# Optimization experiments

Hardware: AMD Instinct MI355X
Metric: run time of the kernel (lower is better)

The kernel has to match this reference:

```python
import jax, jax.numpy as jnp
import numpy as np

VOCAB = 100000
D = 128
B = 256
L = 2048  # leaves per tree (power of two -> complete binary tree)


def setup_inputs() -> dict:
    key = jax.random.key(0)
    k1, k2, k3, k4 = jax.random.split(key, 4)
    word_ids = jax.random.randint(k1, (B, L), 0, VOCAB)
    embedding = jax.random.normal(k2, (VOCAB, D), dtype=jnp.float32) * 0.1
    # torch nn.Linear(2*D, D): weight [D, 2*D], bias [D]
    W = jax.random.normal(k3, (D, 2 * D), dtype=jnp.float32) * (1.0 / np.sqrt(2 * D))
    b = jax.random.normal(k4, (D,), dtype=jnp.float32) * 0.01
    return {"word_ids": word_ids, "embedding": embedding, "W": W, "b": b}


def reference(word_ids, embedding, W, b):
    # Leaves: embedding lookup for every leaf of every tree. [B, L, D]
    x = embedding[word_ids]
    # Internal nodes, batched by depth: each level combines adjacent pairs
    # via linear(concat(left, right)). log2(L) levels (static unroll).
    while x.shape[1] > 1:
        left = x[:, 0::2, :]   # [B, n/2, D]
        right = x[:, 1::2, :]  # [B, n/2, D]
        pair = jnp.concatenate([left, right], axis=-1)  # [B, n/2, 2D]
        x = jnp.einsum('bnd,od->bno', pair, W) + b      # [B, n/2, D]
    return x[:, 0, :]  # root result per tree, [B, D]
```

## Files before the change

kernel.cpp:

```cpp
#include <hip/hip_runtime.h>


typedef __bf16 bf16x8 __attribute__((ext_vector_type(8)));
typedef float f32x4 __attribute__((ext_vector_type(4)));

#define STRIDE 136

__device__ __forceinline__ unsigned short bf16rne(float x) {
    union { float f; unsigned int u; } v; v.f = x;
    unsigned int u = v.u;
    u += 0x7fffu + ((u >> 16) & 1u);
    return (unsigned short)(u >> 16);
}

__global__ void pack_w_kernel(const float* __restrict__ W,
                              unsigned short* __restrict__ wpack) {
    const int f = blockIdx.x;
    const int tid = threadIdx.x;
    const int wv = tid >> 6, l = tid & 63;
    const int nl = f >> 3, kk = f & 7;
    const int o = ((wv << 1) + nl) * 16 + (l & 15);
    const int d = kk * 32 + ((l >> 4) << 3);
    const float* src = W + o * 256 + d;
    unsigned short h[8];
#pragma unroll
    for (int j = 0; j < 8; ++j) h[j] = bf16rne(src[j]);
    uint4* dst = (uint4*)(wpack + (size_t)(f * 256 + tid) * 8);
    *dst = *(const uint4*)h;
}

__global__ __launch_bounds__(256) void tree64_kernel(
    const int* __restrict__ wid, const float* __restrict__ emb,
    const unsigned short* __restrict__ wpack, const float* __restrict__ bias,
    unsigned short* __restrict__ yout)
{
    __shared__ __align__(16) unsigned short buf[2][64 * STRIDE];
    __shared__ int ids[64];
    const int tid = threadIdx.x;
    const int blk = blockIdx.x;
    const int batch = blk >> 5;
    const int sub = blk & 31;
    const int wv = tid >> 6;
    const int ln = tid & 63;
    const int q = ln >> 4;
    const int lm = ln & 15;

    if (tid < 64) ids[tid] = wid[batch * 2048 + sub * 64 + tid];

    bf16x8 wf[16];
    const bf16x8* wp = (const bf16x8*)wpack;
#pragma unroll
    for (int f = 0; f < 16; ++f) wf[f] = wp[f * 256 + tid];

    float bval[2];
    bval[0] = bias[(2 * wv + 0) * 16 + lm];
    bval[1] = bias[(2 * wv + 1) * 16 + lm];

    __syncthreads();

#pragma unroll
    for (int i = 0; i < 8; ++i) {
        const int flat = tid + 256 * i;
        const int row = flat >> 5;
        const int c4 = flat & 31;
        const float4 v = *(const float4*)(emb + (size_t)ids[row] * 128 + c4 * 4);
        ushort4 h;
        h.x = bf16rne(v.x); h.y = bf16rne(v.y);
        h.z = bf16rne(v.z); h.w = bf16rne(v.w);
        *(ushort4*)&buf[0][row * STRIDE + c4 * 4] = h;
    }
    __syncthreads();

    int nin = 64;
    int rb = 0;
    while (nin > 1) {
        const int nout = nin >> 1;
        const int ntm = (nout + 15) >> 4;
        for (int mt = 0; mt < ntm; ++mt) {
            const int m = mt * 16 + lm;
            bf16x8 af[8];
#pragma unroll
            for (int kk = 0; kk < 8; ++kk) {
                const int k = kk * 32 + q * 8;
                const int row = 2 * m + (k >> 7);
                const int col = k & 127;
                af[kk] = *(const bf16x8*)&buf[rb][row * STRIDE + col];
            }
#pragma unroll
            for (int nl = 0; nl < 2; ++nl) {
                f32x4 acc = { bval[nl], bval[nl], bval[nl], bval[nl] };
#pragma unroll
                for (int kk = 0; kk < 8; ++kk)
                    acc = __builtin_amdgcn_mfma_f32_16x16x32_bf16(
                        af[kk], wf[nl * 8 + kk], acc, 0, 0, 0);
                const int col = (2 * wv + nl) * 16 + lm;
                if (nout == 1) {
                    if (q == 0)
                        yout[(size_t)(batch * 32 + sub) * 128 + col] =
                            bf16rne(acc[0]);
                } else {
#pragma unroll
                    for (int r = 0; r < 4; ++r) {
                        const int row = mt * 16 + q * 4 + r;
                        if (row < nout)
                            buf[rb ^ 1][row * STRIDE + col] = bf16rne(acc[r]);
                    }
                }
            }
        }
        __syncthreads();
        rb ^= 1;
        nin = nout;
    }
}

__global__ __launch_bounds__(256) void tree32_kernel(
    const unsigned short* __restrict__ yin,
    const unsigned short* __restrict__ wpack, const float* __restrict__ bias,
    float* __restrict__ out)
{
    __shared__ __align__(16) unsigned short buf[2][32 * STRIDE];
    const int tid = threadIdx.x;
    const int batch = blockIdx.x;
    const int wv = tid >> 6, ln = tid & 63, q = ln >> 4, lm = ln & 15;

    bf16x8 wf[16];
    const bf16x8* wp = (const bf16x8*)wpack;
#pragma unroll
    for (int f = 0; f < 16; ++f) wf[f] = wp[f * 256 + tid];
    float bval[2];
    bval[0] = bias[(2 * wv + 0) * 16 + lm];
    bval[1] = bias[(2 * wv + 1) * 16 + lm];

#pragma unroll
    for (int i = 0; i < 2; ++i) {
        const int flat = tid + 256 * i;
        const int row = flat >> 4;
        const int c8 = flat & 15;
        const bf16x8 v =
            *(const bf16x8*)(yin + (size_t)(batch * 32 + row) * 128 + c8 * 8);
        *(bf16x8*)&buf[0][row * STRIDE + c8 * 8] = v;
    }
    __syncthreads();

    int nin = 32, rb = 0;
    while (nin > 1) {
        const int nout = nin >> 1;
        const int m = lm;
        bf16x8 af[8];
#pragma unroll
        for (int kk = 0; kk < 8; ++kk) {
            const int k = kk * 32 + q * 8;
            const int row = 2 * m + (k >> 7);
            const int col = k & 127;
            af[kk] = *(const bf16x8*)&buf[rb][row * STRIDE + col];
        }
#pragma unroll
        for (int nl = 0; nl < 2; ++nl) {
            f32x4 acc = { bval[nl], bval[nl], bval[nl], bval[nl] };
#pragma unroll
            for (int kk = 0; kk < 8; ++kk)
                acc = __builtin_amdgcn_mfma_f32_16x16x32_bf16(
                    af[kk], wf[nl * 8 + kk], acc, 0, 0, 0);
            const int col = (2 * wv + nl) * 16 + lm;
            if (nout == 1) {
                if (q == 0) out[(size_t)batch * 128 + col] = acc[0];
            } else {
#pragma unroll
                for (int r = 0; r < 4; ++r) {
                    const int row = q * 4 + r;
                    if (row < nout)
                        buf[rb ^ 1][row * STRIDE + col] = bf16rne(acc[r]);
                }
            }
        }
        __syncthreads();
        rb ^= 1;
        nin = nout;
    }
}

extern "C" void kernel_launch(void* const* d_in, const int* in_sizes, int n_in,
                              void* d_out, int out_size, void* d_ws, size_t ws_size,
                              hipStream_t stream) {
    const int*   wid = (const int*)d_in[0];
    const float* emb = (const float*)d_in[1];
    const float* W   = (const float*)d_in[2];
    const float* b   = (const float*)d_in[3];
    float* out = (float*)d_out;

    unsigned short* wpack = (unsigned short*)d_ws;
    unsigned short* y     = wpack + 32768;

    pack_w_kernel<<<16, 256, 0, stream>>>(W, wpack);
    tree64_kernel<<<8192, 256, 0, stream>>>(wid, emb, wpack, b, y);
    tree32_kernel<<<256, 256, 0, stream>>>(y, wpack, b, out);
}
```

Before: 149.9 us.

## Pre-convert embedding table to bf16 and gather half-width rows

Adds a prep kernel that converts the whole fp32 embedding table to bf16 in workspace, and folds the W packing into the same launch. The leaf gather in tree64 then reads 256-byte bf16 rows instead of 512-byte fp32 rows, halving gather traffic. The manual bit-twiddling round-to-nearest-even is replaced with native bf16 vector conversions. The cost is an extra streaming pass over the full table on every call, and a fallback fp32 path is kept for when the workspace is too small.

```diff
diff --git a/kernel.cpp b/kernel.cpp
--- a/kernel.cpp
+++ b/kernel.cpp
@@ -2,19 +2,38 @@
 
 
 typedef __bf16 bf16x8 __attribute__((ext_vector_type(8)));
+typedef __bf16 bf16x4 __attribute__((ext_vector_type(4)));
 typedef float f32x4 __attribute__((ext_vector_type(4)));
+typedef float f32x8 __attribute__((ext_vector_type(8)));
 
 #define STRIDE 136
 
-__device__ __forceinline__ unsigned short bf16rne(float x) {
-    union { float f; unsigned int u; } v; v.f = x;
-    unsigned int u = v.u;
-    u += 0x7fffu + ((u >> 16) & 1u);
-    return (unsigned short)(u >> 16);
+__global__ __launch_bounds__(256) void prep_kernel(
+    const float* __restrict__ W, const float* __restrict__ emb,
+    __bf16* __restrict__ wpack, __bf16* __restrict__ ebf)
+{
+    const int tid = threadIdx.x;
+    const int blk = blockIdx.x;
+    if (blk < 16) {
+        const int f = blk;
+        const int wv = tid >> 6, l = tid & 63;
+        const int nl = f >> 3, kk = f & 7;
+        const int o = ((wv << 1) + nl) * 16 + (l & 15);
+        const int d = kk * 32 + ((l >> 4) << 3);
+        const float* src = W + o * 256 + d;
+        bf16x8 h;
+#pragma unroll
+        for (int j = 0; j < 8; ++j) h[j] = (__bf16)src[j];
+        *(bf16x8*)(wpack + (size_t)(f * 256 + tid) * 8) = h;
+    } else {
+        const size_t base = ((size_t)(blk - 16) * 256 + tid) * 8;
+        const f32x8 v = *(const f32x8*)(emb + base);
+        *(bf16x8*)(ebf + base) = __builtin_convertvector(v, bf16x8);
+    }
 }
 
 __global__ void pack_w_kernel(const float* __restrict__ W,
-                              unsigned short* __restrict__ wpack) {
+                              __bf16* __restrict__ wpack) {
     const int f = blockIdx.x;
     const int tid = threadIdx.x;
     const int wv = tid >> 6, l = tid & 63;
@@ -22,57 +41,17 @@
     const int o = ((wv << 1) + nl) * 16 + (l & 15);
     const int d = kk * 32 + ((l >> 4) << 3);
     const float* src = W + o * 256 + d;
-    unsigned short h[8];
-#pragma unroll
-    for (int j = 0; j < 8; ++j) h[j] = bf16rne(src[j]);
-    uint4* dst = (uint4*)(wpack + (size_t)(f * 256 + tid) * 8);
-    *dst = *(const uint4*)h;
-}
-
-__global__ __launch_bounds__(256) void tree64_kernel(
-    const int* __restrict__ wid, const float* __restrict__ emb,
-    const unsigned short* __restrict__ wpack, const float* __restrict__ bias,
-    unsigned short* __restrict__ yout)
-{
-    __shared__ __align__(16) unsigned short buf[2][64 * STRIDE];
-    __shared__ int ids[64];
-    const int tid = threadIdx.x;
-    const int blk = blockIdx.x;
-    const int batch = blk >> 5;
-    const int sub = blk & 31;
-    const int wv = tid >> 6;
-    const int ln = tid & 63;
-    const int q = ln >> 4;
-    const int lm = ln & 15;
-
-    if (tid < 64) ids[tid] = wid[batch * 2048 + sub * 64 + tid];
-
-    bf16x8 wf[16];
-    const bf16x8* wp = (const bf16x8*)wpack;
-#pragma unroll
-    for (int f = 0; f < 16; ++f) wf[f] = wp[f * 256 + tid];
-
-    float bval[2];
-    bval[0] = bias[(2 * wv + 0) * 16 + lm];
-    bval[1] = bias[(2 * wv + 1) * 16 + lm];
-
-    __syncthreads();
-
-#pragma unroll
-    for (int i = 0; i < 8; ++i) {
-        const int flat = tid + 256 * i;
-        const int row = flat >> 5;
-        const int c4 = flat & 31;
-        const float4 v = *(const float4*)(emb + (size_t)ids[row] * 128 + c4 * 4);
-        ushort4 h;
-        h.x = bf16rne(v.x); h.y = bf16rne(v.y);
-        h.z = bf16rne(v.z); h.w = bf16rne(v.w);
-        *(ushort4*)&buf[0][row * STRIDE + c4 * 4] = h;
-    }
-    __syncthreads();
-
-    int nin = 64;
-    int rb = 0;
+    bf16x8 h;
+#pragma unroll
+    for (int j = 0; j < 8; ++j) h[j] = (__bf16)src[j];
+    *(bf16x8*)(wpack + (size_t)(f * 256 + tid) * 8) = h;
+}
+
+__device__ __forceinline__ void tree64_levels(
+    __bf16 (*buf)[64 * STRIDE], const bf16x8* wf, const float* bval,
+    int wv, int q, int lm, __bf16* yrow)
+{
+    int nin = 64, rb = 0;
     while (nin > 1) {
         const int nout = nin >> 1;
         const int ntm = (nout + 15) >> 4;
@@ -95,15 +74,14 @@
                         af[kk], wf[nl * 8 + kk], acc, 0, 0, 0);
                 const int col = (2 * wv + nl) * 16 + lm;
                 if (nout == 1) {
-                    if (q == 0)
-                        yout[(size_t)(batch * 32 + sub) * 128 + col] =
-                            bf16rne(acc[0]);
+                    if (q == 0) yrow[col] = (__bf16)acc[0];
                 } else {
+                    const bf16x4 hv = __builtin_convertvector(acc, bf16x4);
 #pragma unroll
                     for (int r = 0; r < 4; ++r) {
                         const int row = mt * 16 + q * 4 + r;
                         if (row < nout)
-                            buf[rb ^ 1][row * STRIDE + col] = bf16rne(acc[r]);
+                            buf[rb ^ 1][row * STRIDE + col] = hv[r];
                     }
                 }
             }
@@ -114,12 +92,88 @@
     }
 }
 
+__global__ __launch_bounds__(256) void tree64_kernel(
+    const int* __restrict__ wid, const __bf16* __restrict__ ebf,
+    const __bf16* __restrict__ wpack, const float* __restrict__ bias,
+    __bf16* __restrict__ yout)
+{
+    __shared__ __align__(16) __bf16 buf[2][64 * STRIDE];
+    __shared__ int ids[64];
+    const int tid = threadIdx.x;
+    const int batch = blockIdx.x >> 5;
+    const int sub = blockIdx.x & 31;
+    const int wv = tid >> 6, ln = tid & 63, q = ln >> 4, lm = ln & 15;
+
+    if (tid < 64) ids[tid] = wid[batch * 2048 + sub * 64 + tid];
+
+    bf16x8 wf[16];
+    const bf16x8* wp = (const bf16x8*)wpack;
+#pragma unroll
+    for (int f = 0; f < 16; ++f) wf[f] = wp[f * 256 + tid];
+    float bval[2];
+    bval[0] = bias[(2 * wv + 0) * 16 + lm];
+    bval[1] = bias[(2 * wv + 1) * 16 + lm];
+
+    __syncthreads();
+
+#pragma unroll
+    for (int i = 0; i < 4; ++i) {
+        const int flat = tid + 256 * i;
+        const int row = flat >> 4;
+        const int c8 = flat & 15;
+        const bf16x8 v = *(const bf16x8*)(ebf + (size_t)ids[row] * 128 + c8 * 8);
+        *(bf16x8*)&buf[0][row * STRIDE + c8 * 8] = v;
+    }
+    __syncthreads();
+
+    tree64_levels(buf, wf, bval, wv, q, lm,
+                  yout + (size_t)(batch * 32 + sub) * 128);
+}
+
+__global__ __launch_bounds__(256) void tree64_f32_kernel(
+    const int* __restrict__ wid, const float* __restrict__ emb,
+    const __bf16* __restrict__ wpack, const float* __restrict__ bias,
+    __bf16* __restrict__ yout)
+{
+    __shared__ __align__(16) __bf16 buf[2][64 * STRIDE];
+    __shared__ int ids[64];
+    const int tid = threadIdx.x;
+    const int batch = blockIdx.x >> 5;
+    const int sub = blockIdx.x & 31;
+    const int wv = tid >> 6, ln = tid & 63, q = ln >> 4, lm = ln & 15;
+
+    if (tid < 64) ids[tid] = wid[batch * 2048 + sub * 64 + tid];
+
+    bf16x8 wf[16];
+    const bf16x8* wp = (const bf16x8*)wpack;
+#pragma unroll
+    for (int f = 0; f < 16; ++f) wf[f] = wp[f * 256 + tid];
+    float bval[2];
+    bval[0] = bias[(2 * wv + 0) * 16 + lm];
+    bval[1] = bias[(2 * wv + 1) * 16 + lm];
+
+    __syncthreads();
+
+#pragma unroll
+    for (int i = 0; i < 8; ++i) {
+        const int flat = tid + 256 * i;
+        const int row = flat >> 5;
+        const int c4 = flat & 31;
+        const f32x4 v = *(const f32x4*)(emb + (size_t)ids[row] * 128 + c4 * 4);
+        *(bf16x4*)&buf[0][row * STRIDE + c4 * 4] =
+            __builtin_convertvector(v, bf16x4);
+    }
+    __syncthreads();
+
+    tree64_levels(buf, wf, bval, wv, q, lm,
+                  yout + (size_t)(batch * 32 + sub) * 128);
+}
+
 __global__ __launch_bounds__(256) void tree32_kernel(
-    const unsigned short* __restrict__ yin,
-    const unsigned short* __restrict__ wpack, const float* __restrict__ bias,
-    float* __restrict__ out)
-{
-    __shared__ __align__(16) unsigned short buf[2][32 * STRIDE];
+    const __bf16* __restrict__ yin, const __bf16* __restrict__ wpack,
+    const float* __restrict__ bias, float* __restrict__ out)
+{
+    __shared__ __align__(16) __bf16 buf[2][32 * STRIDE];
     const int tid = threadIdx.x;
     const int batch = blockIdx.x;
     const int wv = tid >> 6, ln = tid & 63, q = ln >> 4, lm = ln & 15;
@@ -166,11 +220,12 @@
             if (nout == 1) {
                 if (q == 0) out[(size_t)batch * 128 + col] = acc[0];
             } else {
+                const bf16x4 hv = __builtin_convertvector(acc, bf16x4);
 #pragma unroll
                 for (int r = 0; r < 4; ++r) {
                     const int row = q * 4 + r;
                     if (row < nout)
-                        buf[rb ^ 1][row * STRIDE + col] = bf16rne(acc[r]);
+                        buf[rb ^ 1][row * STRIDE + col] = hv[r];
                 }
             }
         }
@@ -189,10 +244,19 @@
     const float* b   = (const float*)d_in[3];
     float* out = (float*)d_out;
 
-    unsigned short* wpack = (unsigned short*)d_ws;
-    unsigned short* y     = wpack + 32768;
-
-    pack_w_kernel<<<16, 256, 0, stream>>>(W, wpack);
-    tree64_kernel<<<8192, 256, 0, stream>>>(wid, emb, wpack, b, y);
-    tree32_kernel<<<256, 256, 0, stream>>>(y, wpack, b, out);
-}
+    __bf16* wpack = (__bf16*)d_ws;
+    __bf16* ebf   = wpack + 32768;
+    __bf16* y     = ebf + 12800000;
+    const size_t need = (32768 + 12800000 + 256 * 32 * 128) * sizeof(__bf16);
+
+    if (ws_size >= need) {
+        prep_kernel<<<16 + 6250, 256, 0, stream>>>(W, emb, wpack, ebf);
+        tree64_kernel<<<8192, 256, 0, stream>>>(wid, ebf, wpack, b, y);
+        tree32_kernel<<<256, 256, 0, stream>>>(y, wpack, b, out);
+    } else {
+        __bf16* y2 = wpack + 32768;
+        pack_w_kernel<<<16, 256, 0, stream>>>(W, wpack);
+        tree64_f32_kernel<<<8192, 256, 0, stream>>>(wid, emb, wpack, b, y2);
+        tree32_kernel<<<256, 256, 0, stream>>>(y2, wpack, b, out);
+    }
+}
```

After: 146.7 us. 1.02x faster.

## Process 128-leaf subtrees per block with unrolled levels and hardware bf16 conversion

Applied to the files above, without the earlier changes.

Each block now reduces 128 leaves down to two outputs instead of 64 leaves down to one, which halves the grid and so halves the per-block weight-fragment loads and launch overhead. The level loop is fully templated and unrolled, and a custom buffer-reuse schedule fits in less LDS so occupancy can be raised with launch bounds of 3. Word ids are preloaded into registers rather than staged through shared memory, and the manual bf16 rounding is replaced with vector conversions that may map to hardware instructions. Register pressure is higher, and the more intricate buffer aliasing is a correctness risk.

```diff
diff --git a/kernel.cpp b/kernel.cpp
--- a/kernel.cpp
+++ b/kernel.cpp
@@ -2,19 +2,13 @@
 
 
 typedef __bf16 bf16x8 __attribute__((ext_vector_type(8)));
+typedef __bf16 bf16x4 __attribute__((ext_vector_type(4)));
 typedef float f32x4 __attribute__((ext_vector_type(4)));
 
 #define STRIDE 136
 
-__device__ __forceinline__ unsigned short bf16rne(float x) {
-    union { float f; unsigned int u; } v; v.f = x;
-    unsigned int u = v.u;
-    u += 0x7fffu + ((u >> 16) & 1u);
-    return (unsigned short)(u >> 16);
-}
-
 __global__ void pack_w_kernel(const float* __restrict__ W,
-                              unsigned short* __restrict__ wpack) {
+                              __bf16* __restrict__ wpack) {
     const int f = blockIdx.x;
     const int tid = threadIdx.x;
     const int wv = tid >> 6, l = tid & 63;
@@ -22,104 +16,129 @@
     const int o = ((wv << 1) + nl) * 16 + (l & 15);
     const int d = kk * 32 + ((l >> 4) << 3);
     const float* src = W + o * 256 + d;
-    unsigned short h[8];
-#pragma unroll
-    for (int j = 0; j < 8; ++j) h[j] = bf16rne(src[j]);
-    uint4* dst = (uint4*)(wpack + (size_t)(f * 256 + tid) * 8);
-    *dst = *(const uint4*)h;
-}
-
-__global__ __launch_bounds__(256) void tree64_kernel(
+    bf16x8 h;
+#pragma unroll
+    for (int j = 0; j < 8; ++j) h[j] = (__bf16)src[j];
+    *(bf16x8*)(wpack + (size_t)(f * 256 + tid) * 8) = h;
+}
+
+template <int NOUT>
+__device__ __forceinline__ void level_step(
+    const __bf16* src0, const __bf16* src1, __bf16* dst,
+    const bf16x8* wf, const float* bval, int wv, int q, int lm)
+{
+    const int ntm = (NOUT + 15) >> 4;
+#pragma unroll
+    for (int mt = 0; mt < ntm; ++mt) {
+        const __bf16* src = mt ? src1 : src0;
+        const int me = (NOUT >= 16) ? lm : (lm < NOUT ? lm : 0);
+        bf16x8 af[8];
+#pragma unroll
+        for (int kk = 0; kk < 8; ++kk) {
+            const int hi = kk >> 2;
+            const int col = (kk & 3) * 32 + q * 8;
+            const int row = 2 * me + hi;
+            af[kk] = *(const bf16x8*)&src[row * STRIDE + col];
+        }
+#pragma unroll
+        for (int nl = 0; nl < 2; ++nl) {
+            f32x4 acc = { bval[nl], bval[nl], bval[nl], bval[nl] };
+#pragma unroll
+            for (int kk = 0; kk < 8; ++kk)
+                acc = __builtin_amdgcn_mfma_f32_16x16x32_bf16(
+                    af[kk], wf[nl * 8 + kk], acc, 0, 0, 0);
+            const int col = (2 * wv + nl) * 16 + lm;
+            const bf16x4 hv = __builtin_convertvector(acc, bf16x4);
+#pragma unroll
+            for (int r = 0; r < 4; ++r) {
+                const int row = mt * 16 + q * 4 + r;
+                if (row < NOUT)
+                    dst[row * STRIDE + col] = hv[r];
+            }
+        }
+    }
+    __syncthreads();
+}
+
+__device__ __forceinline__ void level_final(
+    const __bf16* src, __bf16* yrow,
+    const bf16x8* wf, const float* bval, int wv, int q, int lm)
+{
+    const int me = (lm < 2) ? lm : 0;
+    bf16x8 af[8];
+#pragma unroll
+    for (int kk = 0; kk < 8; ++kk) {
+        const int hi = kk >> 2;
+        const int col = (kk & 3) * 32 + q * 8;
+        af[kk] = *(const bf16x8*)&src[(2 * me + hi) * STRIDE + col];
+    }
+#pragma unroll
+    for (int nl = 0; nl < 2; ++nl) {
+        f32x4 acc = { bval[nl], bval[nl], bval[nl], bval[nl] };
+#pragma unroll
+        for (int kk = 0; kk < 8; ++kk)
+            acc = __builtin_amdgcn_mfma_f32_16x16x32_bf16(
+                af[kk], wf[nl * 8 + kk], acc, 0, 0, 0);
+        const int col = (2 * wv + nl) * 16 + lm;
+        if (q == 0) {
+            yrow[0 * 128 + col] = (__bf16)acc[0];
+            yrow[1 * 128 + col] = (__bf16)acc[1];
+        }
+    }
+}
+
+__global__ __launch_bounds__(256, 3) void tree128_kernel(
     const int* __restrict__ wid, const float* __restrict__ emb,
-    const unsigned short* __restrict__ wpack, const float* __restrict__ bias,
-    unsigned short* __restrict__ yout)
-{
-    __shared__ __align__(16) unsigned short buf[2][64 * STRIDE];
-    __shared__ int ids[64];
+    const __bf16* __restrict__ wpack, const float* __restrict__ bias,
+    __bf16* __restrict__ yout)
+{
+    __shared__ __align__(16) __bf16 bufA[128 * STRIDE];
+    __shared__ __align__(16) __bf16 bufB[32 * STRIDE];
     const int tid = threadIdx.x;
-    const int blk = blockIdx.x;
-    const int batch = blk >> 5;
-    const int sub = blk & 31;
-    const int wv = tid >> 6;
-    const int ln = tid & 63;
-    const int q = ln >> 4;
-    const int lm = ln & 15;
-
-    if (tid < 64) ids[tid] = wid[batch * 2048 + sub * 64 + tid];
+    const int batch = blockIdx.x >> 4;
+    const int grp = blockIdx.x & 15;
+    const int wv = tid >> 6, ln = tid & 63, q = ln >> 4, lm = ln & 15;
 
     bf16x8 wf[16];
     const bf16x8* wp = (const bf16x8*)wpack;
 #pragma unroll
     for (int f = 0; f < 16; ++f) wf[f] = wp[f * 256 + tid];
-
     float bval[2];
     bval[0] = bias[(2 * wv + 0) * 16 + lm];
     bval[1] = bias[(2 * wv + 1) * 16 + lm];
 
+    const int* wb = wid + batch * 2048 + grp * 128;
+    int idreg[16];
+#pragma unroll
+    for (int i = 0; i < 16; ++i) idreg[i] = wb[(tid >> 5) + 8 * i];
+
+#pragma unroll
+    for (int i = 0; i < 16; ++i) {
+        const int row = (tid >> 5) + 8 * i;
+        const int c4 = tid & 31;
+        const f32x4 v = *(const f32x4*)(emb + (size_t)idreg[i] * 128 + c4 * 4);
+        *(bf16x4*)&bufA[row * STRIDE + c4 * 4] =
+            __builtin_convertvector(v, bf16x4);
+    }
     __syncthreads();
 
-#pragma unroll
-    for (int i = 0; i < 8; ++i) {
-        const int flat = tid + 256 * i;
-        const int row = flat >> 5;
-        const int c4 = flat & 31;
-        const float4 v = *(const float4*)(emb + (size_t)ids[row] * 128 + c4 * 4);
-        ushort4 h;
-        h.x = bf16rne(v.x); h.y = bf16rne(v.y);
-        h.z = bf16rne(v.z); h.w = bf16rne(v.w);
-        *(ushort4*)&buf[0][row * STRIDE + c4 * 4] = h;
-    }
-    __syncthreads();
-
-    int nin = 64;
-    int rb = 0;
-    while (nin > 1) {
-        const int nout = nin >> 1;
-        const int ntm = (nout + 15) >> 4;
-        for (int mt = 0; mt < ntm; ++mt) {
-            const int m = mt * 16 + lm;
-            bf16x8 af[8];
-#pragma unroll
-            for (int kk = 0; kk < 8; ++kk) {
-                const int k = kk * 32 + q * 8;
-                const int row = 2 * m + (k >> 7);
-                const int col = k & 127;
-                af[kk] = *(const bf16x8*)&buf[rb][row * STRIDE + col];
-            }
-#pragma unroll
-            for (int nl = 0; nl < 2; ++nl) {
-                f32x4 acc = { bval[nl], bval[nl], bval[nl], bval[nl] };
-#pragma unroll
-                for (int kk = 0; kk < 8; ++kk)
-                    acc = __builtin_amdgcn_mfma_f32_16x16x32_bf16(
-                        af[kk], wf[nl * 8 + kk], acc, 0, 0, 0);
-                const int col = (2 * wv + nl) * 16 + lm;
-                if (nout == 1) {
-                    if (q == 0)
-                        yout[(size_t)(batch * 32 + sub) * 128 + col] =
-                            bf16rne(acc[0]);
-                } else {
-#pragma unroll
-                    for (int r = 0; r < 4; ++r) {
-                        const int row = mt * 16 + q * 4 + r;
-                        if (row < nout)
-                            buf[rb ^ 1][row * STRIDE + col] = bf16rne(acc[r]);
-                    }
-                }
-            }
-        }
-        __syncthreads();
-        rb ^= 1;
-        nin = nout;
-    }
+    __bf16* A = bufA;
+    __bf16* B = bufB;
+    level_step<32>(A,               A + 32 * STRIDE, B,              wf, bval, wv, q, lm);
+    level_step<32>(A + 64 * STRIDE, A + 96 * STRIDE, A,              wf, bval, wv, q, lm);
+    level_step<32>(B,               A,               A + 32 * STRIDE,wf, bval, wv, q, lm);
+    level_step<16>(A + 32 * STRIDE, nullptr,         B,              wf, bval, wv, q, lm);
+    level_step<8> (B,               nullptr,         A,              wf, bval, wv, q, lm);
+    level_step<4> (A,               nullptr,         B,              wf, bval, wv, q, lm);
+    level_final(B, yout + (size_t)(batch * 32 + grp * 2) * 128,
+                wf, bval, wv, q, lm);
 }
 
 __global__ __launch_bounds__(256) void tree32_kernel(
-    const unsigned short* __restrict__ yin,
-    const unsigned short* __restrict__ wpack, const float* __restrict__ bias,
-    float* __restrict__ out)
-{
-    __shared__ __align__(16) unsigned short buf[2][32 * STRIDE];
+    const __bf16* __restrict__ yin, const __bf16* __restrict__ wpack,
+    const float* __restrict__ bias, float* __restrict__ out)
+{
+    __shared__ __align__(16) __bf16 buf[2][32 * STRIDE];
     const int tid = threadIdx.x;
     const int batch = blockIdx.x;
     const int wv = tid >> 6, ln = tid & 63, q = ln >> 4, lm = ln & 15;
@@ -146,14 +165,13 @@
     int nin = 32, rb = 0;
     while (nin > 1) {
         const int nout = nin >> 1;
-        const int m = lm;
+        const int me = (lm < nout) ? lm : 0;
         bf16x8 af[8];
 #pragma unroll
         for (int kk = 0; kk < 8; ++kk) {
-            const int k = kk * 32 + q * 8;
-            const int row = 2 * m + (k >> 7);
-            const int col = k & 127;
-            af[kk] = *(const bf16x8*)&buf[rb][row * STRIDE + col];
+            const int hi = kk >> 2;
+            const int col = (kk & 3) * 32 + q * 8;
+            af[kk] = *(const bf16x8*)&buf[rb][(2 * me + hi) * STRIDE + col];
         }
 #pragma unroll
         for (int nl = 0; nl < 2; ++nl) {
@@ -166,11 +184,12 @@
             if (nout == 1) {
                 if (q == 0) out[(size_t)batch * 128 + col] = acc[0];
             } else {
+                const bf16x4 hv = __builtin_convertvector(acc, bf16x4);
 #pragma unroll
                 for (int r = 0; r < 4; ++r) {
                     const int row = q * 4 + r;
                     if (row < nout)
-                        buf[rb ^ 1][row * STRIDE + col] = bf16rne(acc[r]);
+                        buf[rb ^ 1][row * STRIDE + col] = hv[r];
                 }
             }
         }
@@ -189,10 +208,10 @@
     const float* b   = (const float*)d_in[3];
     float* out = (float*)d_out;
 
-    unsigned short* wpack = (unsigned short*)d_ws;
-    unsigned short* y     = wpack + 32768;
+    __bf16* wpack = (__bf16*)d_ws;
+    __bf16* y     = wpack + 32768;
 
     pack_w_kernel<<<16, 256, 0, stream>>>(W, wpack);
-    tree64_kernel<<<8192, 256, 0, stream>>>(wid, emb, wpack, b, y);
+    tree128_kernel<<<4096, 256, 0, stream>>>(wid, emb, wpack, b, y);
     tree32_kernel<<<256, 256, 0, stream>>>(y, wpack, b, out);
 }
```

Result: faster. 130.9 us (-12.7%).
